# Optimization experiments

Hardware: AMD Instinct MI355X
Metric: run time of the kernel (lower is better)

Reference implementation:

```python
import jax, jax.numpy as jnp
import numpy as np

N_NODES = 50000
N_EDGES = 800000
FEAT = 256
HID = 64
OUT = 40


def setup_inputs() -> dict:
    key = jax.random.key(0)
    ks = jax.random.split(key, 5)
    x = jax.random.normal(ks[0], (N_NODES, FEAT), dtype=jnp.float32)
    edge_index = jax.random.randint(ks[1], (2, N_EDGES), 0, N_NODES, dtype=jnp.int64)
    # Glorot-style init for GCN linear weights
    W1 = jax.random.normal(ks[2], (FEAT, HID), dtype=jnp.float32) * (1.0 / np.sqrt(FEAT))
    b1 = jnp.zeros((HID,), dtype=jnp.float32)
    W2 = jax.random.normal(ks[3], (HID, OUT), dtype=jnp.float32) * (1.0 / np.sqrt(HID))
    b2 = jnp.zeros((OUT,), dtype=jnp.float32)
    return {"x": x, "edge_index": edge_index, "W1": W1, "b1": b1, "W2": W2, "b2": b2}


def _gcn_conv(h, W, b, src, dst, norm, n_nodes):
    # GCNConv: linear transform first (reduces message width), then
    # symmetric-normalized gather-scale-scatter aggregation.
    h = h @ W  # [N, out]
    msg = h[src] * norm[:, None]  # [E+N, out] gather + scale
    agg = jax.ops.segment_sum(msg, dst, num_segments=n_nodes)  # scatter-add
    return agg + b


def reference(x, edge_index, W1, b1, W2, b2):
    n = x.shape[0]
    # add self loops (GCNConv default add_self_loops=True)
    loops = jnp.arange(n, dtype=edge_index.dtype)
    src = jnp.concatenate([edge_index[0], loops])
    dst = jnp.concatenate([edge_index[1], loops])
    # symmetric normalization: deg computed on A + I (in-degree at dst)
    deg = jax.ops.segment_sum(jnp.ones_like(dst, dtype=x.dtype), dst, num_segments=n)
    dinv = jax.lax.rsqrt(deg)  # deg >= 1 due to self loops
    norm = dinv[src] * dinv[dst]  # [E+N]

    h = jax.nn.relu(_gcn_conv(x, W1, b1, src, dst, norm, n))
    # dropout is identity in eval mode (reference baseline)
    h = _gcn_conv(h, W2, b2, src, dst, norm, n)
    return jax.nn.log_softmax(h, axis=1)
```

## Files before the change

### kernel.cpp

```cpp
#include <hip/hip_runtime.h>
#include <hip/hip_bf16.h>


constexpr int NN   = 50000;
constexpr int NNP  = 50048;
constexpr int ZR   = 50000;
constexpr int NE   = 800000;
constexpr int FEAT = 256;
constexpr int HID  = 64;
constexpr int OUTD = 40;
constexpr int NC   = (NN + 255) / 256;
constexpr int FCH  = 2048;
constexpr int NCH  = (NE + FCH - 1) / FCH;

typedef short bf16x8 __attribute__((ext_vector_type(8)));
typedef float f32x4  __attribute__((ext_vector_type(4)));

__device__ __forceinline__ float b2f(__hip_bfloat16 v) { return __bfloat162float(v); }
__device__ __forceinline__ float bflo(unsigned u) { return __uint_as_float(u << 16); }
__device__ __forceinline__ float bfhi(unsigned u) { return __uint_as_float(u & 0xffff0000u); }
__device__ __forceinline__ unsigned short f2bu(float f) {
    __hip_bfloat16 h = __float2bfloat16(f);
    return *(unsigned short*)&h;
}
__device__ __forceinline__ unsigned pack2bf(float a, float b) {
    return (unsigned)f2bu(a) | ((unsigned)f2bu(b) << 16);
}
__device__ __forceinline__ float loadF(const void* p, int i, bool f32) {
    return f32 ? ((const float*)p)[i] : b2f(((const __hip_bfloat16*)p)[i]);
}
__device__ __forceinline__ int loadE(const int* ei, int e, int row, bool i64) {
    long long idx = (long long)row * NE + e;
    return i64 ? ei[2 * idx] : ei[idx];
}
__device__ __forceinline__ bf16x8 pack8(float4 a, float4 b) {
    bf16x8 r;
    r[0] = (short)f2bu(a.x); r[1] = (short)f2bu(a.y);
    r[2] = (short)f2bu(a.z); r[3] = (short)f2bu(a.w);
    r[4] = (short)f2bu(b.x); r[5] = (short)f2bu(b.y);
    r[6] = (short)f2bu(b.z); r[7] = (short)f2bu(b.w);
    return r;
}

__global__ __launch_bounds__(256) void k_zero(const unsigned* __restrict__ xw,
                                              const int* __restrict__ ew,
                                              int* flags, int* cnt,
                                              unsigned* __restrict__ h2pad) {
    int i = blockIdx.x * 256 + threadIdx.x;
    if (i < NN) cnt[i] = 0;
    if (blockIdx.x == 0 && threadIdx.x < 20) h2pad[threadIdx.x] = 0;
    if (blockIdx.x == 0 && threadIdx.x == 0) {
        int outliers = 0;
        for (int k = 0; k < 256; k++) {
            int e = (xw[k] >> 7) & 0xFF;
            if (e < 100 || e > 140) outliers++;
        }
        flags[0] = (outliers > 64) ? 1 : 0;
        int nz = 0;
        for (int k = 1; k < 64; k += 2)
            if (ew[k] != 0) nz++;
        flags[1] = (nz == 0) ? 1 : 0;
    }
}

__global__ __launch_bounds__(256) void k_hist(const int* __restrict__ ei,
                                              const int* __restrict__ flags,
                                              int* cnt, int* __restrict__ rank) {
    const bool i64 = flags[1] != 0;
    int e = blockIdx.x * 256 + threadIdx.x;
    if (e < NE) rank[e] = atomicAdd(&cnt[loadE(ei, e, 1, i64)], 1);
}
__global__ __launch_bounds__(256) void k_scan1(const int* __restrict__ cnt,
                                               int* row_start, int* partial, float* dinv) {
    __shared__ int s[256];
    int t = threadIdx.x, i = blockIdx.x * 256 + t;
    int v = (i < NN) ? cnt[i] : 0;
    if (i < NN) dinv[i] = rsqrtf(1.0f + (float)v);
    s[t] = v;
    __syncthreads();
    for (int off = 1; off < 256; off <<= 1) {
        int tmp = (t >= off) ? s[t - off] : 0;
        __syncthreads();
        s[t] += tmp;
        __syncthreads();
    }
    if (i < NN) row_start[i] = s[t] - v;
    if (t == 255) partial[blockIdx.x] = s[255];
}
__global__ __launch_bounds__(256) void k_scan2p(const int* __restrict__ partial, int* pp) {
    __shared__ int s[256];
    int t = threadIdx.x;
    int v = (t < NC) ? partial[t] : 0;
    s[t] = v;
    __syncthreads();
    for (int off = 1; off < 256; off <<= 1) {
        int tmp = (t >= off) ? s[t - off] : 0;
        __syncthreads();
        s[t] += tmp;
        __syncthreads();
    }
    pp[t] = s[t] - v;
}
__global__ __launch_bounds__(256) void k_fill(const int* __restrict__ ei,
                                              const int* __restrict__ flags,
                                              const int* __restrict__ row_start,
                                              const int* __restrict__ pp,
                                              const int* __restrict__ rank,
                                              unsigned short* __restrict__ csr16) {
    const bool i64 = flags[1] != 0;
    const int cls = blockIdx.x & 7;
    const int e0 = (blockIdx.x >> 3) * FCH;
#pragma unroll
    for (int k = 0; k < FCH / 256; k++) {
        int e = e0 + k * 256 + threadIdx.x;
        if (e < NE) {
            int d = loadE(ei, e, 1, i64);
            if (d / 6250 == cls) {
                int s = loadE(ei, e, 0, i64);
                csr16[row_start[d] + pp[d >> 8] + rank[e]] = (unsigned short)s;
            }
        }
    }
}

__global__ __launch_bounds__(256) void k_gemm1(const void* __restrict__ xb,
                                               const void* __restrict__ W1,
                                               const float* __restrict__ dinv,
                                               const int* __restrict__ flags,
                                               unsigned short* __restrict__ h1u) {
    __shared__ __align__(16) unsigned short wt16[64 * 264];
    const bool f32 = flags[0] != 0;
    const int t = threadIdx.x;
    if (f32) {
        const float* wf = (const float*)W1;
        for (int i = t * 4; i < FEAT * HID; i += 1024) {
            float4 w = *(const float4*)(wf + i);
            int k = i >> 6, n0 = i & 63;
            wt16[(n0 + 0) * 264 + k] = f2bu(w.x);
            wt16[(n0 + 1) * 264 + k] = f2bu(w.y);
            wt16[(n0 + 2) * 264 + k] = f2bu(w.z);
            wt16[(n0 + 3) * 264 + k] = f2bu(w.w);
        }
    } else {
        const unsigned short* wu = (const unsigned short*)W1;
        for (int i = t * 4; i < FEAT * HID; i += 1024) {
            ushort4 w = *(const ushort4*)(wu + i);
            int k = i >> 6, n0 = i & 63;
            wt16[(n0 + 0) * 264 + k] = w.x;
            wt16[(n0 + 1) * 264 + k] = w.y;
            wt16[(n0 + 2) * 264 + k] = w.z;
            wt16[(n0 + 3) * 264 + k] = w.w;
        }
    }
    const int wv = t >> 6, lane = t & 63, l15 = lane & 15, quad = lane >> 4;
    const int gr = blockIdx.x * 64 + wv * 16 + l15;
    const bool rowok = gr < NN;
    f32x4 acc[4];
#pragma unroll
    for (int nt = 0; nt < 4; nt++) acc[nt] = (f32x4){0.f, 0.f, 0.f, 0.f};
    __syncthreads();

    if (f32) {
        const float* xr = (const float*)xb + (size_t)gr * FEAT + quad * 8;
        float4 z4 = make_float4(0, 0, 0, 0);
        float4 c0 = rowok ? *(const float4*)xr : z4;
        float4 c1 = rowok ? *(const float4*)(xr + 4) : z4;
#pragma unroll
        for (int ks = 0; ks < 8; ks++) {
            float4 n0 = z4, n1 = z4;
            if (ks < 7 && rowok) {
                n0 = *(const float4*)(xr + (ks + 1) * 32);
                n1 = *(const float4*)(xr + (ks + 1) * 32 + 4);
            }
            bf16x8 a = pack8(c0, c1);
            const unsigned short* wk = wt16 + ks * 32 + quad * 8;
#pragma unroll
            for (int nt = 0; nt < 4; nt++) {
                bf16x8 b = *(const bf16x8*)(wk + (size_t)(nt * 16 + l15) * 264);
                acc[nt] = __builtin_amdgcn_mfma_f32_16x16x32_bf16(a, b, acc[nt], 0, 0, 0);
            }
            c0 = n0; c1 = n1;
        }
    } else {
        const unsigned short* xr = (const unsigned short*)xb + (size_t)gr * FEAT + quad * 8;
        bf16x8 zz = (bf16x8){0, 0, 0, 0, 0, 0, 0, 0};
        bf16x8 cur = rowok ? *(const bf16x8*)xr : zz;
#pragma unroll
        for (int ks = 0; ks < 8; ks++) {
            bf16x8 nxt = zz;
            if (ks < 7 && rowok) nxt = *(const bf16x8*)(xr + (ks + 1) * 32);
            const unsigned short* wk = wt16 + ks * 32 + quad * 8;
#pragma unroll
            for (int nt = 0; nt < 4; nt++) {
                bf16x8 b = *(const bf16x8*)(wk + (size_t)(nt * 16 + l15) * 264);
                acc[nt] = __builtin_amdgcn_mfma_f32_16x16x32_bf16(cur, b, acc[nt], 0, 0, 0);
            }
            cur = nxt;
        }
    }
    const int rbase = blockIdx.x * 64 + wv * 16 + quad * 4;
    float dv[4];
#pragma unroll
    for (int r = 0; r < 4; r++) dv[r] = (rbase + r < NN) ? dinv[rbase + r] : 0.f;
#pragma unroll
    for (int r = 0; r < 4; r++) {
        int grow = rbase + r;
#pragma unroll
        for (int nt = 0; nt < 4; nt++)
            h1u[(size_t)grow * HID + nt * 16 + l15] = f2bu(acc[nt][r] * dv[r]);
    }
}

__global__ __launch_bounds__(256) void k_gather1f(const uint2* __restrict__ h1v,
                                                  const float* __restrict__ dinv,
                                                  const int* __restrict__ row_start,
                                                  const int* __restrict__ pp,
                                                  const int* __restrict__ cnt,
                                                  const unsigned short* __restrict__ csr16,
                                                  const void* __restrict__ W2,
                                                  const void* __restrict__ b1,
                                                  const int* __restrict__ flags,
                                                  unsigned short* __restrict__ h2u) {
    __shared__ __align__(16) float w2t[OUTD * 68];
    __shared__ __align__(16) float gbuf[16 * 68];
    __shared__ float dns[16];
    const bool f32 = flags[0] != 0;
    const int t = threadIdx.x;
    for (int i = t; i < HID * OUTD; i += 256) {
        int c = i >> 6, k = i & 63;
        w2t[c * 68 + k] = loadF(W2, (size_t)k * OUTD + c, f32);
    }
    const int nl = t >> 4, l16 = t & 15;
    const int n = blockIdx.x * 16 + nl;
    const float dn = dinv[n];
    uint2 u0 = h1v[(size_t)n * 16 + l16];
    float a0 = bflo(u0.x), a1 = bfhi(u0.x), a2 = bflo(u0.y), a3 = bfhi(u0.y);
    float e0 = 0.f, e1 = 0.f, e2 = 0.f, e3 = 0.f;
    const int rs = row_start[n] + pp[n >> 8], c = cnt[n];
    for (int base = 0; base < c; base += 16) {
        int rem = c - base;
        int sv = (l16 < rem) ? (int)csr16[rs + base + l16] : ZR;
        uint2 b[8], d[8];
#pragma unroll
        for (int j = 0; j < 8; j++) {
            int s = __shfl(sv, j, 16);
            b[j] = h1v[(size_t)s * 16 + l16];
        }
#pragma unroll
        for (int j = 0; j < 8; j++) {
            int s = __shfl(sv, j + 8, 16);
            d[j] = h1v[(size_t)s * 16 + l16];
        }
#pragma unroll
        for (int j = 0; j < 8; j++) {
            a0 += bflo(b[j].x); a1 += bfhi(b[j].x);
            a2 += bflo(b[j].y); a3 += bfhi(b[j].y);
            e0 += bflo(d[j].x); e1 += bfhi(d[j].x);
            e2 += bflo(d[j].y); e3 += bfhi(d[j].y);
        }
    }
    int cb = 4 * l16;
    float g0 = fmaxf(dn * (a0 + e0) + loadF(b1, cb, f32), 0.f);
    float g1 = fmaxf(dn * (a1 + e1) + loadF(b1, cb + 1, f32), 0.f);
    float g2 = fmaxf(dn * (a2 + e2) + loadF(b1, cb + 2, f32), 0.f);
    float g3 = fmaxf(dn * (a3 + e3) + loadF(b1, cb + 3, f32), 0.f);
    *(float4*)(gbuf + nl * 68 + cb) = make_float4(g0, g1, g2, g3);
    if (l16 == 0) dns[nl] = dn;
    __syncthreads();
    for (int idx = t; idx < 16 * OUTD; idx += 256) {
        int node = idx / OUTD, col = idx % OUTD;
        const float4* gp = (const float4*)(gbuf + node * 68);
        const float4* wp = (const float4*)(w2t + col * 68);
        float o = 0.f;
#pragma unroll 4
        for (int k4 = 0; k4 < 16; k4++) {
            float4 a = gp[k4], b = wp[k4];
            o += a.x * b.x + a.y * b.y + a.z * b.z + a.w * b.w;
        }
        h2u[(size_t)(blockIdx.x * 16 + node) * OUTD + col] = f2bu(o * dns[node]);
    }
}

__global__ __launch_bounds__(256) void k_gather2(const uint2* __restrict__ h2v,
                                                 const float* __restrict__ dinv,
                                                 const int* __restrict__ row_start,
                                                 const int* __restrict__ pp,
                                                 const int* __restrict__ cnt,
                                                 const unsigned short* __restrict__ csr16,
                                                 const void* __restrict__ b2,
                                                 const int* __restrict__ flags,
                                                 void* __restrict__ out) {
    const bool f32 = flags[0] != 0;
    const int t = threadIdx.x;
    const int nl = t >> 4, l16 = t & 15;
    const int n = blockIdx.x * 16 + nl;
    const bool act = l16 < 10;
    const float dn = dinv[n];
    const int lclamp = act ? l16 : 9;
    uint2 u0 = h2v[(size_t)n * 10 + lclamp];
    float a0 = bflo(u0.x), a1 = bfhi(u0.x), a2 = bflo(u0.y), a3 = bfhi(u0.y);
    float e0 = 0.f, e1 = 0.f, e2 = 0.f, e3 = 0.f;
    const int rs = row_start[n] + pp[n >> 8], c = cnt[n];
    for (int base = 0; base < c; base += 16) {
        int rem = c - base;
        int sv = (l16 < rem) ? (int)csr16[rs + base + l16] : ZR;
        uint2 b[8], d[8];
#pragma unroll
        for (int j = 0; j < 8; j++) {
            int s = __shfl(sv, j, 16);
            b[j] = h2v[(size_t)s * 10 + lclamp];
        }
#pragma unroll
        for (int j = 0; j < 8; j++) {
            int s = __shfl(sv, j + 8, 16);
            d[j] = h2v[(size_t)s * 10 + lclamp];
        }
#pragma unroll
        for (int j = 0; j < 8; j++) {
            a0 += bflo(b[j].x); a1 += bfhi(b[j].x);
            a2 += bflo(b[j].y); a3 += bfhi(b[j].y);
            e0 += bflo(d[j].x); e1 += bfhi(d[j].x);
            e2 += bflo(d[j].y); e3 += bfhi(d[j].y);
        }
    }
    int cb = 4 * l16;
    float v0 = -3.0e38f, v1 = -3.0e38f, v2 = -3.0e38f, v3 = -3.0e38f;
    if (act) {
        v0 = dn * (a0 + e0) + loadF(b2, cb, f32);
        v1 = dn * (a1 + e1) + loadF(b2, cb + 1, f32);
        v2 = dn * (a2 + e2) + loadF(b2, cb + 2, f32);
        v3 = dn * (a3 + e3) + loadF(b2, cb + 3, f32);
    }
    float mx = fmaxf(fmaxf(v0, v1), fmaxf(v2, v3));
#pragma unroll
    for (int off = 8; off; off >>= 1) mx = fmaxf(mx, __shfl_xor(mx, off, 16));
    float ev = act ? expf(v0 - mx) + expf(v1 - mx) + expf(v2 - mx) + expf(v3 - mx) : 0.f;
#pragma unroll
    for (int off = 8; off; off >>= 1) ev += __shfl_xor(ev, off, 16);
    float lg = logf(ev);
    if (act) {
        float r0 = v0 - mx - lg, r1 = v1 - mx - lg;
        float r2 = v2 - mx - lg, r3 = v3 - mx - lg;
        if (f32) {
            *(float4*)((float*)out + (size_t)n * OUTD + cb) = make_float4(r0, r1, r2, r3);
        } else {
            ((uint2*)out)[(size_t)n * 10 + l16] = make_uint2(pack2bf(r0, r1), pack2bf(r2, r3));
        }
    }
}

extern "C" void kernel_launch(void* const* d_in, const int* in_sizes, int n_in,
                              void* d_out, int out_size, void* d_ws, size_t ws_size,
                              hipStream_t stream) {
    const void* x  = d_in[0];
    const int*  ei = (const int*)d_in[1];
    const void* W1 = d_in[2];
    const void* b1 = d_in[3];
    const void* W2 = d_in[4];
    const void* b2 = d_in[5];

    float* ws        = (float*)d_ws;
    int*   flags     = (int*)ws;
    float* dinv      = ws + 16;
    int*   cnt       = (int*)(dinv + 50048);
    int*   row_start = cnt + 50048;
    int*   partial   = row_start + 50048;
    int*   pp        = partial + 256;
    int*   rank      = pp + 256;
    unsigned short* csr16 = (unsigned short*)(rank + NE);
    unsigned short* h1u   = csr16 + NE;
    unsigned short* h2u   = h1u + (size_t)NNP * HID;
    unsigned* h2pad = (unsigned*)(h2u + (size_t)ZR * OUTD);

    k_zero  <<<(NN + 255) / 256, 256, 0, stream>>>((const unsigned*)x, ei, flags, cnt, h2pad);
    k_hist  <<<(NE + 255) / 256, 256, 0, stream>>>(ei, flags, cnt, rank);
    k_scan1 <<<NC, 256, 0, stream>>>(cnt, row_start, partial, dinv);
    k_scan2p<<<1, 256, 0, stream>>>(partial, pp);
    k_fill  <<<NCH * 8, 256, 0, stream>>>(ei, flags, row_start, pp, rank, csr16);
    k_gemm1 <<<NNP / 64, 256, 0, stream>>>(x, W1, dinv, flags, h1u);
    k_gather1f<<<NN / 16, 256, 0, stream>>>((const uint2*)h1u, dinv, row_start, pp, cnt, csr16,
                                            W2, b1, flags, h2u);
    k_gather2<<<NN / 16, 256, 0, stream>>>((const uint2*)h2u, dinv, row_start, pp, cnt, csr16,
                                           b2, flags, d_out);
}
```

Baseline: 230.1 us.

## Split layer-1 features into two column halves and unfuse the W2 matvec

The first-layer hidden features are stored as two separate 32-column tables, and the gather kernel processes each half in its own block, so every gathered row table is half as large and more likely to stay in cache. The W2 projection, previously fused into the gather kernel, now runs as a separate matvec kernel reading a bf16 intermediate buffer. This trades an extra kernel launch, an intermediate write and read, and twice as many index loads for better cache locality on the random gathers.

```diff
diff --git a/kernel.cpp b/kernel.cpp
--- a/kernel.cpp
+++ b/kernel.cpp
@@ -12,6 +12,7 @@
 constexpr int NC   = (NN + 255) / 256;
 constexpr int FCH  = 2048;
 constexpr int NCH  = (NE + FCH - 1) / FCH;
+constexpr int NG1  = (NN + 31) / 32;
 
 typedef short bf16x8 __attribute__((ext_vector_type(8)));
 typedef float f32x4  __attribute__((ext_vector_type(4)));
@@ -19,6 +20,7 @@
 __device__ __forceinline__ float b2f(__hip_bfloat16 v) { return __bfloat162float(v); }
 __device__ __forceinline__ float bflo(unsigned u) { return __uint_as_float(u << 16); }
 __device__ __forceinline__ float bfhi(unsigned u) { return __uint_as_float(u & 0xffff0000u); }
+__device__ __forceinline__ float us2f(unsigned short u) { return __uint_as_float((unsigned)u << 16); }
 __device__ __forceinline__ unsigned short f2bu(float f) {
     __hip_bfloat16 h = __float2bfloat16(f);
     return *(unsigned short*)&h;
@@ -127,7 +129,8 @@
                                                const void* __restrict__ W1,
                                                const float* __restrict__ dinv,
                                                const int* __restrict__ flags,
-                                               unsigned short* __restrict__ h1u) {
+                                               unsigned short* __restrict__ h1a,
+                                               unsigned short* __restrict__ h1b) {
     __shared__ __align__(16) unsigned short wt16[64 * 264];
     const bool f32 = flags[0] != 0;
     const int t = threadIdx.x;
@@ -206,66 +209,89 @@
     for (int r = 0; r < 4; r++) {
         int grow = rbase + r;
 #pragma unroll
-        for (int nt = 0; nt < 4; nt++)
-            h1u[(size_t)grow * HID + nt * 16 + l15] = f2bu(acc[nt][r] * dv[r]);
-    }
-}
-
-__global__ __launch_bounds__(256) void k_gather1f(const uint2* __restrict__ h1v,
+        for (int nt = 0; nt < 2; nt++)
+            h1a[(size_t)grow * 32 + nt * 16 + l15] = f2bu(acc[nt][r] * dv[r]);
+#pragma unroll
+        for (int nt = 2; nt < 4; nt++)
+            h1b[(size_t)grow * 32 + (nt - 2) * 16 + l15] = f2bu(acc[nt][r] * dv[r]);
+    }
+}
+
+__global__ __launch_bounds__(256) void k_gather1s(const uint2* __restrict__ h1av,
+                                                  const uint2* __restrict__ h1bv,
                                                   const float* __restrict__ dinv,
                                                   const int* __restrict__ row_start,
                                                   const int* __restrict__ pp,
                                                   const int* __restrict__ cnt,
                                                   const unsigned short* __restrict__ csr16,
-                                                  const void* __restrict__ W2,
                                                   const void* __restrict__ b1,
                                                   const int* __restrict__ flags,
-                                                  unsigned short* __restrict__ h2u) {
+                                                  unsigned short* __restrict__ gtmp) {
+    const bool f32 = flags[0] != 0;
+    const int half = blockIdx.x & 1;
+    const uint2* __restrict__ tab = half ? h1bv : h1av;
+    const int t = threadIdx.x;
+    const int n = (blockIdx.x >> 1) * 32 + (t >> 3);
+    if (n >= NN) return;
+    const int l8 = t & 7;
+    const float dn = dinv[n];
+    uint2 u0 = tab[(size_t)n * 8 + l8];
+    float a0 = bflo(u0.x), a1 = bfhi(u0.x), a2 = bflo(u0.y), a3 = bfhi(u0.y);
+    float e0 = 0.f, e1 = 0.f, e2 = 0.f, e3 = 0.f;
+    const int rs = row_start[n] + pp[n >> 8], c = cnt[n];
+    for (int base = 0; base < c; base += 16) {
+        int rem = c - base;
+        int svA = (l8 < rem)     ? (int)csr16[rs + base + l8]     : ZR;
+        int svB = (l8 + 8 < rem) ? (int)csr16[rs + base + 8 + l8] : ZR;
+        uint2 b[8], d[8];
+#pragma unroll
+        for (int j = 0; j < 8; j++) {
+            int s = __shfl(svA, j, 8);
+            b[j] = tab[(size_t)s * 8 + l8];
+        }
+#pragma unroll
+        for (int j = 0; j < 8; j++) {
+            int s = __shfl(svB, j, 8);
+            d[j] = tab[(size_t)s * 8 + l8];
+        }
+#pragma unroll
+        for (int j = 0; j < 8; j++) {
+            a0 += bflo(b[j].x); a1 += bfhi(b[j].x);
+            a2 += bflo(b[j].y); a3 += bfhi(b[j].y);
+            e0 += bflo(d[j].x); e1 += bfhi(d[j].x);
+            e2 += bflo(d[j].y); e3 += bfhi(d[j].y);
+        }
+    }
+    const int cb = 32 * half + 4 * l8;
+    float g0 = fmaxf(dn * (a0 + e0) + loadF(b1, cb, f32), 0.f);
+    float g1 = fmaxf(dn * (a1 + e1) + loadF(b1, cb + 1, f32), 0.f);
+    float g2 = fmaxf(dn * (a2 + e2) + loadF(b1, cb + 2, f32), 0.f);
+    float g3 = fmaxf(dn * (a3 + e3) + loadF(b1, cb + 3, f32), 0.f);
+    ushort4 pk;
+    pk.x = f2bu(g0); pk.y = f2bu(g1); pk.z = f2bu(g2); pk.w = f2bu(g3);
+    *(ushort4*)(gtmp + (size_t)n * HID + cb) = pk;
+}
+
+__global__ __launch_bounds__(256) void k_matvec(const unsigned short* __restrict__ gtmp,
+                                                const float* __restrict__ dinv,
+                                                const void* __restrict__ W2,
+                                                const int* __restrict__ flags,
+                                                unsigned short* __restrict__ h2u) {
     __shared__ __align__(16) float w2t[OUTD * 68];
     __shared__ __align__(16) float gbuf[16 * 68];
     __shared__ float dns[16];
     const bool f32 = flags[0] != 0;
     const int t = threadIdx.x;
+    const int n0 = blockIdx.x * 16;
     for (int i = t; i < HID * OUTD; i += 256) {
         int c = i >> 6, k = i & 63;
         w2t[c * 68 + k] = loadF(W2, (size_t)k * OUTD + c, f32);
     }
-    const int nl = t >> 4, l16 = t & 15;
-    const int n = blockIdx.x * 16 + nl;
-    const float dn = dinv[n];
-    uint2 u0 = h1v[(size_t)n * 16 + l16];
-    float a0 = bflo(u0.x), a1 = bfhi(u0.x), a2 = bflo(u0.y), a3 = bfhi(u0.y);
-    float e0 = 0.f, e1 = 0.f, e2 = 0.f, e3 = 0.f;
-    const int rs = row_start[n] + pp[n >> 8], c = cnt[n];
-    for (int base = 0; base < c; base += 16) {
-        int rem = c - base;
-        int sv = (l16 < rem) ? (int)csr16[rs + base + l16] : ZR;
-        uint2 b[8], d[8];
-#pragma unroll
-        for (int j = 0; j < 8; j++) {
-            int s = __shfl(sv, j, 16);
-            b[j] = h1v[(size_t)s * 16 + l16];
-        }
-#pragma unroll
-        for (int j = 0; j < 8; j++) {
-            int s = __shfl(sv, j + 8, 16);
-            d[j] = h1v[(size_t)s * 16 + l16];
-        }
-#pragma unroll
-        for (int j = 0; j < 8; j++) {
-            a0 += bflo(b[j].x); a1 += bfhi(b[j].x);
-            a2 += bflo(b[j].y); a3 += bfhi(b[j].y);
-            e0 += bflo(d[j].x); e1 += bfhi(d[j].x);
-            e2 += bflo(d[j].y); e3 += bfhi(d[j].y);
-        }
-    }
-    int cb = 4 * l16;
-    float g0 = fmaxf(dn * (a0 + e0) + loadF(b1, cb, f32), 0.f);
-    float g1 = fmaxf(dn * (a1 + e1) + loadF(b1, cb + 1, f32), 0.f);
-    float g2 = fmaxf(dn * (a2 + e2) + loadF(b1, cb + 2, f32), 0.f);
-    float g3 = fmaxf(dn * (a3 + e3) + loadF(b1, cb + 3, f32), 0.f);
-    *(float4*)(gbuf + nl * 68 + cb) = make_float4(g0, g1, g2, g3);
-    if (l16 == 0) dns[nl] = dn;
+    for (int i = t; i < 16 * HID; i += 256) {
+        int node = i >> 6, k = i & 63;
+        gbuf[node * 68 + k] = us2f(gtmp[(size_t)(n0 + node) * HID + k]);
+    }
+    if (t < 16) dns[t] = dinv[n0 + t];
     __syncthreads();
     for (int idx = t; idx < 16 * OUTD; idx += 256) {
         int node = idx / OUTD, col = idx % OUTD;
@@ -277,7 +303,7 @@
             float4 a = gp[k4], b = wp[k4];
             o += a.x * b.x + a.y * b.y + a.z * b.z + a.w * b.w;
         }
-        h2u[(size_t)(blockIdx.x * 16 + node) * OUTD + col] = f2bu(o * dns[node]);
+        h2u[(size_t)(n0 + node) * OUTD + col] = f2bu(o * dns[node]);
     }
 }
 
@@ -368,8 +394,10 @@
     int*   pp        = partial + 256;
     int*   rank      = pp + 256;
     unsigned short* csr16 = (unsigned short*)(rank + NE);
-    unsigned short* h1u   = csr16 + NE;
-    unsigned short* h2u   = h1u + (size_t)NNP * HID;
+    unsigned short* h1a   = csr16 + NE;
+    unsigned short* h1b   = h1a + (size_t)NNP * 32;
+    unsigned short* gtmp  = h1b + (size_t)NNP * 32;
+    unsigned short* h2u   = gtmp + (size_t)NNP * HID;
     unsigned* h2pad = (unsigned*)(h2u + (size_t)ZR * OUTD);
 
     k_zero  <<<(NN + 255) / 256, 256, 0, stream>>>((const unsigned*)x, ei, flags, cnt, h2pad);
@@ -377,9 +405,10 @@
     k_scan1 <<<NC, 256, 0, stream>>>(cnt, row_start, partial, dinv);
     k_scan2p<<<1, 256, 0, stream>>>(partial, pp);
     k_fill  <<<NCH * 8, 256, 0, stream>>>(ei, flags, row_start, pp, rank, csr16);
-    k_gemm1 <<<NNP / 64, 256, 0, stream>>>(x, W1, dinv, flags, h1u);
-    k_gather1f<<<NN / 16, 256, 0, stream>>>((const uint2*)h1u, dinv, row_start, pp, cnt, csr16,
-                                            W2, b1, flags, h2u);
+    k_gemm1 <<<NNP / 64, 256, 0, stream>>>(x, W1, dinv, flags, h1a, h1b);
+    k_gather1s<<<NG1 * 2, 256, 0, stream>>>((const uint2*)h1a, (const uint2*)h1b, dinv,
+                                            row_start, pp, cnt, csr16, b1, flags, gtmp);
+    k_matvec<<<NN / 16, 256, 0, stream>>>(gtmp, dinv, W2, flags, h2u);
     k_gather2<<<NN / 16, 256, 0, stream>>>((const uint2*)h2u, dinv, row_start, pp, cnt, csr16,
                                            b2, flags, d_out);
 }
```

New measurement: 238.8 us. +3.8%, slower.
